# Performance work log

Hardware: AMD Instinct MI355X
Metric: run time of the kernel (lower is better)

Reference implementation:

```python
import jax, jax.numpy as jnp
import numpy as np
from jax import lax

EPS = 1e-8


def setup_inputs() -> dict:
    key = jax.random.key(0)
    ks = jax.random.split(key, 8)
    B, Cin, Cout, Wd, H, Wi, K = 16, 512, 512, 512, 64, 64, 3
    x = jax.random.normal(ks[0], (B, Cin, H, Wi), dtype=jnp.float32)
    w = jax.random.normal(ks[1], (B, Wd), dtype=jnp.float32)
    noise = jax.random.normal(ks[2], (B, 1, H, Wi), dtype=jnp.float32)
    # EqualizedLinear params (weight stored as N(0,1), runtime scale 1/sqrt(w_dim)); bias init 1.0
    w_style = jax.random.normal(ks[3], (Cin, Wd), dtype=jnp.float32)
    b_style = jnp.ones((Cin,), dtype=jnp.float32)
    # ConvModLayer equalized weight, stored N(0,1), runtime scale 1/sqrt(Cin*K*K)
    w_conv = jax.random.normal(ks[4], (Cout, Cin, K, K), dtype=jnp.float32)
    scale_noise = 0.1 * jax.random.normal(ks[5], (1,), dtype=jnp.float32)
    bias = 0.1 * jax.random.normal(ks[6], (Cout,), dtype=jnp.float32)
    return {"x": x, "w": w, "noise": noise, "w_style": w_style, "b_style": b_style,
            "w_conv": w_conv, "scale_noise": scale_noise, "bias": bias}


def reference(x, w, noise, w_style, b_style, w_conv, scale_noise, bias):
    B, Cin, H, W = x.shape
    Cout, _, K, _ = w_conv.shape
    # to_style: equalized linear, A = w @ (w_style / sqrt(w_dim)).T + b_style
    c_lin = 1.0 / jnp.sqrt(jnp.float32(w_style.shape[1]))
    A = w @ (w_style * c_lin).T + b_style  # [B, Cin]
    # modulated conv (equalized conv weight scale)
    c_conv = 1.0 / jnp.sqrt(jnp.float32(Cin * K * K))
    wts = (w_conv * c_conv)[None] * A[:, None, :, None, None]  # [B, Cout, Cin, K, K]
    demod = lax.rsqrt(jnp.sum(wts * wts, axis=(2, 3, 4), keepdims=True) + EPS)
    wts = wts * demod
    # grouped-conv batch trick: groups = B
    xg = x.reshape(1, B * Cin, H, W)
    wg = wts.reshape(B * Cout, Cin, K, K)
    out = lax.conv_general_dilated(xg, wg, (1, 1), 'SAME',
                                   feature_group_count=B,
                                   dimension_numbers=('NCHW', 'OIHW', 'NCHW'))
    out = out.reshape(B, Cout, H, W)
    out = out + scale_noise[None, :, None, None] * noise
    out = out + bias[None, :, None, None]
    return jnp.where(out >= 0, out, 0.2 * out)  # LeakyReLU(0.2)
```

## Files before the change

### kernel.cpp

```cpp
#include <hip/hip_runtime.h>
#include <stdint.h>


typedef __attribute__((ext_vector_type(8))) short s16x8;
typedef __attribute__((ext_vector_type(4))) float f32x4;

constexpr int CIN = 512, COUT = 512, WD = 512, HW = 4096;
constexpr float C_LIN  = 0.04419417382415922f;
constexpr float C_CONV = 0.014731391274719739f;
constexpr float CC2    = 1.0f / 4608.0f;

constexpr size_t WS_A = 0, WS_S = 32768, WS_DM = 1081344;
constexpr size_t WS_WP = 1310720, WS_XT = 6291456;

__device__ __forceinline__ unsigned short f2bf(float f) {
  union { float f; unsigned int u; } v; v.f = f;
  unsigned int u = v.u + 0x7FFFu + ((v.u >> 16) & 1u);
  return (unsigned short)(u >> 16);
}

__device__ __forceinline__ void gload16(const void* g, void* l) {
  __builtin_amdgcn_global_load_lds((const __attribute__((address_space(1))) void*)g,
                                   (__attribute__((address_space(3))) void*)l, 16, 0, 0);
}

__global__ void k_style(const float* __restrict__ w, const float* __restrict__ wsty,
                        const float* __restrict__ bs, float* __restrict__ A) {
  __shared__ float wl[WD];
  __shared__ float red[256];
  const int ci0 = blockIdx.x * 64, b = blockIdx.y, tid = threadIdx.x;
  for (int i = tid; i < WD; i += 256) wl[i] = w[b * WD + i];
  __syncthreads();
  const int ci_l = tid & 63, part = tid >> 6;
  const float4* row = (const float4*)(wsty + (size_t)(ci0 + ci_l) * WD + part * 128);
  float acc = 0.f;
#pragma unroll
  for (int k = 0; k < 32; ++k) {
    float4 v = row[k];
    acc += v.x * wl[part*128 + 4*k] + v.y * wl[part*128 + 4*k+1]
         + v.z * wl[part*128 + 4*k+2] + v.w * wl[part*128 + 4*k+3];
  }
  red[tid] = acc;
  __syncthreads();
  if (part == 0)
    A[b * CIN + ci0 + ci_l] =
        (red[ci_l] + red[64+ci_l] + red[128+ci_l] + red[192+ci_l]) * C_LIN + bs[ci0 + ci_l];
}

__global__ void k_s2(const float* __restrict__ w_conv, float* __restrict__ S) {
  const int co = blockIdx.x, ci = threadIdx.x;
  const float* p = w_conv + ((size_t)co * CIN + ci) * 9;
  float s = 0.f;
#pragma unroll
  for (int t = 0; t < 9; ++t) { float v = p[t]; s += v * v; }
  S[co * CIN + ci] = s;
}

__global__ void k_demod(const float* __restrict__ S, const float* __restrict__ A,
                        float* __restrict__ dm) {
  __shared__ float a2[CIN];
  __shared__ float red[256];
  const int co0 = blockIdx.x * 32, b = blockIdx.y, tid = threadIdx.x;
  for (int i = tid; i < CIN; i += 256) { float a = A[b * CIN + i]; a2[i] = a * a; }
  __syncthreads();
  const int co_l = tid & 31, part = tid >> 5;
  const float4* row = (const float4*)(S + (size_t)(co0 + co_l) * CIN + part * 64);
  float acc = 0.f;
#pragma unroll
  for (int k = 0; k < 16; ++k) {
    float4 v = row[k];
    acc += v.x * a2[part*64 + 4*k] + v.y * a2[part*64 + 4*k+1]
         + v.z * a2[part*64 + 4*k+2] + v.w * a2[part*64 + 4*k+3];
  }
  red[tid] = acc;
  __syncthreads();
  if (tid < 32) {
    float s_ = 0.f;
#pragma unroll
    for (int p = 0; p < 8; ++p) s_ += red[p * 32 + tid];
    dm[b * COUT + co0 + tid] = rsqrtf(CC2 * s_ + 1e-8f);
  }
}

__global__ void k_wpack(const float* __restrict__ wc, uint4* __restrict__ wp) {
  __shared__ float wt[64][289];
  const int ct = blockIdx.x, ch = blockIdx.y, tid = threadIdx.x;
  const int co0 = ct * 64, ci0 = ch * 32;
  for (int i = tid; i < 64 * 288; i += 256) {
    int co = i / 288, r = i - co * 288;
    wt[co][r] = wc[(size_t)(co0 + co) * 4608 + (size_t)ci0 * 9 + r];
  }
  __syncthreads();
  uint4* seg = wp + (size_t)(ct * 16 + ch) * 2304;
  for (int c = tid; c < 2304; c += 256) {
    int t = c >> 8, rem = c & 255, s = rem >> 6, co = rem & 63;
    union { unsigned short u[8]; uint4 v; } pk;
#pragma unroll
    for (int j = 0; j < 8; ++j) pk.u[j] = f2bf(wt[co][(s*8 + j) * 9 + t] * C_CONV);
    seg[c] = pk.v;
  }
}

__global__ void k_xt(const float* __restrict__ x, const float* __restrict__ A,
                     uint4* __restrict__ xt) {
  __shared__ float tile[32][132];
  __shared__ float As[32];
  const int ch = blockIdx.x, b = blockIdx.y, tid = threadIdx.x;
  const int ci0 = ch * 32;
  if (tid < 32) As[tid] = A[b * CIN + ci0 + tid];
  uint4* dst = xt + (size_t)(b * 16 + ch) * 16896;
  for (int i = tid; i < 256; i += 256) {
    int row = i >> 2, s = i & 3;
    uint4 z = {0, 0, 0, 0};
    dst[(row * 4 + s) * 66] = z;
    dst[(row * 4 + s) * 66 + 65] = z;
  }
  __syncthreads();
  for (int pt = 0; pt < 32; ++pt) {
    for (int i = tid; i < 4096; i += 256) {
      int ci = i >> 7, px = i & 127;
      tile[ci][px] = x[((size_t)(b * CIN + ci0 + ci)) * HW + pt * 128 + px] * As[ci];
    }
    __syncthreads();
    for (int c2 = tid; c2 < 512; c2 += 256) {
      int s = c2 >> 7, px = c2 & 127, rl = px >> 6, col = px & 63, row = pt * 2 + rl;
      union { unsigned short u[8]; uint4 v; } pk;
#pragma unroll
      for (int j = 0; j < 8; ++j) pk.u[j] = f2bf(tile[s*8 + j][px]);
      dst[(row * 4 + s) * 66 + 1 + col] = pk.v;
    }
    __syncthreads();
  }
}

__global__ __launch_bounds__(512, 4) void k_conv(
    const uint4* __restrict__ xt, const uint4* __restrict__ wp,
    const float* __restrict__ demod, const float* __restrict__ noise,
    const float* __restrict__ sn_, const float* __restrict__ bias,
    float* __restrict__ out) {

  __shared__ __align__(16) uint4 x_lds[2640];
  __shared__ __align__(16) uint4 w_lds[2304];
  __shared__ float dm_l[64], bi_l[64];

  const int sp = blockIdx.x, ct = blockIdx.y, b = blockIdx.z;
  const int r0 = sp * 8, co0 = ct * 64;
  const int tid = threadIdx.x, lane = tid & 63, wave = tid >> 6;
  const int l15 = lane & 15, l4 = lane >> 4;

  if (tid < 64) dm_l[tid] = demod[b * COUT + co0 + tid];
  else if (tid < 128) bi_l[tid - 64] = bias[co0 + tid - 64];
  if (sp == 0) for (int i = tid; i < 264; i += 512) x_lds[i] = (uint4){0, 0, 0, 0};
  if (sp == 7) for (int i = tid; i < 264; i += 512) x_lds[2376 + i] = (uint4){0, 0, 0, 0};

  const int lo = (r0 - 1 > 0) ? r0 - 1 : 0;
  const int hi = (r0 + 8 < 63) ? r0 + 8 : 63;
  const int cells = (hi - lo + 1) * 264;
  const int dst0 = (lo - (r0 - 1)) * 264;
  const int nI = cells >> 6, tail = cells & 63;

  f32x4 acc[4][4];
#pragma unroll
  for (int m = 0; m < 4; ++m)
#pragma unroll
    for (int f = 0; f < 4; ++f) acc[m][f] = (f32x4){0.f, 0.f, 0.f, 0.f};
  __syncthreads();

  for (int ch = 0; ch < 16; ++ch) {
    const uint4* xsrc = xt + ((size_t)(b * 16 + ch) * 64 + lo) * 264;
    const uint4* wsrc = wp + (size_t)(ct * 16 + ch) * 2304;
    for (int i = wave; i < nI; i += 8)
      gload16(xsrc + i * 64 + lane, &x_lds[dst0 + i * 64]);
    if (tid < tail) x_lds[dst0 + nI * 64 + tid] = xsrc[nI * 64 + tid];
    for (int i = wave; i < 36; i += 8)
      gload16(wsrc + i * 64 + lane, &w_lds[i * 64]);
    __syncthreads();

#pragma unroll
    for (int t = 0; t < 9; ++t) {
      const int dh = t / 3, dw = t - dh * 3;
      s16x8 afr[4], bfr[4];
#pragma unroll
      for (int m = 0; m < 4; ++m)
        afr[m] = *(const s16x8*)&w_lds[(t * 4 + l4) * 64 + m * 16 + l15];
#pragma unroll
      for (int f = 0; f < 4; ++f)
        bfr[f] = *(const s16x8*)&x_lds[((wave + dh) * 4 + l4) * 66 + f * 16 + l15 + dw];
#pragma unroll
      for (int m = 0; m < 4; ++m)
#pragma unroll
        for (int f = 0; f < 4; ++f)
          acc[m][f] = __builtin_amdgcn_mfma_f32_16x16x32_bf16(afr[m], bfr[f], acc[m][f], 0, 0, 0);
    }
    __syncthreads();
  }

  const float sn = sn_[0];
  const int row = r0 + wave;
  float nz[4];
#pragma unroll
  for (int f = 0; f < 4; ++f) nz[f] = sn * noise[b * HW + row * 64 + f * 16 + l15];
#pragma unroll
  for (int m = 0; m < 4; ++m) {
#pragma unroll
    for (int reg = 0; reg < 4; ++reg) {
      const int co_l = m * 16 + l4 * 4 + reg;
      const float d = dm_l[co_l], bv = bi_l[co_l];
      float* op = out + ((size_t)(b * COUT + co0 + co_l)) * HW + row * 64;
#pragma unroll
      for (int f = 0; f < 4; ++f) {
        float v = d * acc[m][f][reg] + nz[f] + bv;
        op[f * 16 + l15] = (v >= 0.f) ? v : 0.2f * v;
      }
    }
  }
}

extern "C" void kernel_launch(void* const* d_in, const int* in_sizes, int n_in,
                              void* d_out, int out_size, void* d_ws, size_t ws_size,
                              hipStream_t stream) {
  (void)in_sizes; (void)n_in; (void)out_size; (void)ws_size;
  const float* x           = (const float*)d_in[0];
  const float* w           = (const float*)d_in[1];
  const float* noise       = (const float*)d_in[2];
  const float* w_style     = (const float*)d_in[3];
  const float* b_style     = (const float*)d_in[4];
  const float* w_conv      = (const float*)d_in[5];
  const float* scale_noise = (const float*)d_in[6];
  const float* bias        = (const float*)d_in[7];
  float* out = (float*)d_out;

  char* ws = (char*)d_ws;
  float* A     = (float*)(ws + WS_A);
  float* S     = (float*)(ws + WS_S);
  float* demod = (float*)(ws + WS_DM);
  uint4* wpack = (uint4*)(ws + WS_WP);
  uint4* xt    = (uint4*)(ws + WS_XT);

  k_style<<<dim3(8, 16), 256, 0, stream>>>(w, w_style, b_style, A);
  k_s2<<<512, 512, 0, stream>>>(w_conv, S);
  k_demod<<<dim3(16, 16), 256, 0, stream>>>(S, A, demod);
  k_wpack<<<dim3(8, 16), 256, 0, stream>>>(w_conv, wpack);
  k_xt<<<dim3(16, 16), 256, 0, stream>>>(x, A, xt);
  k_conv<<<dim3(8, 8, 16), 512, 0, stream>>>(xt, wpack, demod, noise, scale_noise, bias, out);
}
```

Measured before the change: 499.5 us.

## Fuse weight sum-of-squares into packing, parallelize x transform, pad weight LDS rows

Merges the per-(co,ci) squared-weight sum into the weight packing kernel so w_conv is read once, removing one launch. Rewrites the x transpose/modulate kernel to use one wave per (batch, channel chunk, row) over 4096 blocks instead of 256 blocks looping over 32 tiles with LDS staging. Pads packed weight rows from 64 to 66 entries so A-fragment LDS reads in the conv use a shifted bank pattern. The padding adds a little LDS and global footprint, and the new x kernel reads x with strided per-channel loads.

```diff
diff --git a/kernel.cpp b/kernel.cpp
--- a/kernel.cpp
+++ b/kernel.cpp
@@ -9,6 +9,8 @@
 constexpr float C_LIN  = 0.04419417382415922f;
 constexpr float C_CONV = 0.014731391274719739f;
 constexpr float CC2    = 1.0f / 4608.0f;
+
+constexpr int WSEG = 2432;
 
 constexpr size_t WS_A = 0, WS_S = 32768, WS_DM = 1081344;
 constexpr size_t WS_WP = 1310720, WS_XT = 6291456;
@@ -47,13 +49,31 @@
         (red[ci_l] + red[64+ci_l] + red[128+ci_l] + red[192+ci_l]) * C_LIN + bs[ci0 + ci_l];
 }
 
-__global__ void k_s2(const float* __restrict__ w_conv, float* __restrict__ S) {
-  const int co = blockIdx.x, ci = threadIdx.x;
-  const float* p = w_conv + ((size_t)co * CIN + ci) * 9;
-  float s = 0.f;
-#pragma unroll
-  for (int t = 0; t < 9; ++t) { float v = p[t]; s += v * v; }
-  S[co * CIN + ci] = s;
+__global__ void k_sw(const float* __restrict__ wc, uint4* __restrict__ wp,
+                     float* __restrict__ S) {
+  __shared__ float wt[64][289];
+  const int ct = blockIdx.x, ch = blockIdx.y, tid = threadIdx.x;
+  const int co0 = ct * 64, ci0 = ch * 32;
+  for (int i = tid; i < 64 * 288; i += 256) {
+    int co = i / 288, r = i - co * 288;
+    wt[co][r] = wc[(size_t)(co0 + co) * 4608 + (size_t)ci0 * 9 + r];
+  }
+  __syncthreads();
+  uint4* seg = wp + (size_t)(ct * 16 + ch) * WSEG;
+  for (int c = tid; c < 2304; c += 256) {
+    int t = c >> 8, rem = c & 255, s = rem >> 6, co = rem & 63;
+    union { unsigned short u[8]; uint4 v; } pk;
+#pragma unroll
+    for (int j = 0; j < 8; ++j) pk.u[j] = f2bf(wt[co][(s*8 + j) * 9 + t] * C_CONV);
+    seg[(t * 4 + s) * 66 + co] = pk.v;
+  }
+  for (int i = tid; i < 2048; i += 256) {
+    int co = i >> 5, ci = i & 31;
+    float s_ = 0.f;
+#pragma unroll
+    for (int t = 0; t < 9; ++t) { float v = wt[co][ci * 9 + t]; s_ += v * v; }
+    S[(size_t)(co0 + co) * CIN + ci0 + ci] = s_;
+  }
 }
 
 __global__ void k_demod(const float* __restrict__ S, const float* __restrict__ A,
@@ -82,54 +102,22 @@
   }
 }
 
-__global__ void k_wpack(const float* __restrict__ wc, uint4* __restrict__ wp) {
-  __shared__ float wt[64][289];
-  const int ct = blockIdx.x, ch = blockIdx.y, tid = threadIdx.x;
-  const int co0 = ct * 64, ci0 = ch * 32;
-  for (int i = tid; i < 64 * 288; i += 256) {
-    int co = i / 288, r = i - co * 288;
-    wt[co][r] = wc[(size_t)(co0 + co) * 4608 + (size_t)ci0 * 9 + r];
-  }
-  __syncthreads();
-  uint4* seg = wp + (size_t)(ct * 16 + ch) * 2304;
-  for (int c = tid; c < 2304; c += 256) {
-    int t = c >> 8, rem = c & 255, s = rem >> 6, co = rem & 63;
-    union { unsigned short u[8]; uint4 v; } pk;
-#pragma unroll
-    for (int j = 0; j < 8; ++j) pk.u[j] = f2bf(wt[co][(s*8 + j) * 9 + t] * C_CONV);
-    seg[c] = pk.v;
-  }
-}
-
 __global__ void k_xt(const float* __restrict__ x, const float* __restrict__ A,
                      uint4* __restrict__ xt) {
-  __shared__ float tile[32][132];
-  __shared__ float As[32];
-  const int ch = blockIdx.x, b = blockIdx.y, tid = threadIdx.x;
-  const int ci0 = ch * 32;
-  if (tid < 32) As[tid] = A[b * CIN + ci0 + tid];
-  uint4* dst = xt + (size_t)(b * 16 + ch) * 16896;
-  for (int i = tid; i < 256; i += 256) {
-    int row = i >> 2, s = i & 3;
-    uint4 z = {0, 0, 0, 0};
-    dst[(row * 4 + s) * 66] = z;
-    dst[(row * 4 + s) * 66 + 65] = z;
-  }
-  __syncthreads();
-  for (int pt = 0; pt < 32; ++pt) {
-    for (int i = tid; i < 4096; i += 256) {
-      int ci = i >> 7, px = i & 127;
-      tile[ci][px] = x[((size_t)(b * CIN + ci0 + ci)) * HW + pt * 128 + px] * As[ci];
-    }
-    __syncthreads();
-    for (int c2 = tid; c2 < 512; c2 += 256) {
-      int s = c2 >> 7, px = c2 & 127, rl = px >> 6, col = px & 63, row = pt * 2 + rl;
-      union { unsigned short u[8]; uint4 v; } pk;
-#pragma unroll
-      for (int j = 0; j < 8; ++j) pk.u[j] = f2bf(tile[s*8 + j][px]);
-      dst[(row * 4 + s) * 66 + 1 + col] = pk.v;
-    }
-    __syncthreads();
+  const int wid = (blockIdx.x << 2) + (threadIdx.x >> 6);
+  const int lane = threadIdx.x & 63;
+  const int row = wid & 63, ch = (wid >> 6) & 15, b = wid >> 10;
+  const float* xb = x + ((size_t)(b * CIN + ch * 32) << 12) + (row << 6) + lane;
+  const float* Ab = A + b * CIN + ch * 32;
+  uint4* dst = xt + (size_t)((b << 4) + ch) * 16896 + (size_t)(row << 2) * 66;
+#pragma unroll
+  for (int s = 0; s < 4; ++s) {
+    union { unsigned short u[8]; uint4 v; } pk;
+#pragma unroll
+    for (int j = 0; j < 8; ++j)
+      pk.u[j] = f2bf(xb[(size_t)(s * 8 + j) << 12] * Ab[s * 8 + j]);
+    dst[s * 66 + 1 + lane] = pk.v;
+    if (lane < 2) dst[s * 66 + lane * 65] = (uint4){0, 0, 0, 0};
   }
 }
 
@@ -140,7 +128,7 @@
     float* __restrict__ out) {
 
   __shared__ __align__(16) uint4 x_lds[2640];
-  __shared__ __align__(16) uint4 w_lds[2304];
+  __shared__ __align__(16) uint4 w_lds[WSEG];
   __shared__ float dm_l[64], bi_l[64];
 
   const int sp = blockIdx.x, ct = blockIdx.y, b = blockIdx.z;
@@ -168,11 +156,11 @@
 
   for (int ch = 0; ch < 16; ++ch) {
     const uint4* xsrc = xt + ((size_t)(b * 16 + ch) * 64 + lo) * 264;
-    const uint4* wsrc = wp + (size_t)(ct * 16 + ch) * 2304;
+    const uint4* wsrc = wp + (size_t)(ct * 16 + ch) * WSEG;
     for (int i = wave; i < nI; i += 8)
       gload16(xsrc + i * 64 + lane, &x_lds[dst0 + i * 64]);
     if (tid < tail) x_lds[dst0 + nI * 64 + tid] = xsrc[nI * 64 + tid];
-    for (int i = wave; i < 36; i += 8)
+    for (int i = wave; i < 38; i += 8)
       gload16(wsrc + i * 64 + lane, &w_lds[i * 64]);
     __syncthreads();
 
@@ -182,7 +170,7 @@
       s16x8 afr[4], bfr[4];
 #pragma unroll
       for (int m = 0; m < 4; ++m)
-        afr[m] = *(const s16x8*)&w_lds[(t * 4 + l4) * 64 + m * 16 + l15];
+        afr[m] = *(const s16x8*)&w_lds[(t * 4 + l4) * 66 + m * 16 + l15];
 #pragma unroll
       for (int f = 0; f < 4; ++f)
         bfr[f] = *(const s16x8*)&x_lds[((wave + dh) * 4 + l4) * 66 + f * 16 + l15 + dw];
@@ -238,9 +226,8 @@
   uint4* xt    = (uint4*)(ws + WS_XT);
 
   k_style<<<dim3(8, 16), 256, 0, stream>>>(w, w_style, b_style, A);
-  k_s2<<<512, 512, 0, stream>>>(w_conv, S);
+  k_sw<<<dim3(8, 16), 256, 0, stream>>>(w_conv, wpack, S);
   k_demod<<<dim3(16, 16), 256, 0, stream>>>(S, A, demod);
-  k_wpack<<<dim3(8, 16), 256, 0, stream>>>(w_conv, wpack);
-  k_xt<<<dim3(16, 16), 256, 0, stream>>>(x, A, xt);
+  k_xt<<<4096, 256, 0, stream>>>(x, A, xt);
   k_conv<<<dim3(8, 8, 16), 512, 0, stream>>>(xt, wpack, demod, noise, scale_noise, bias, out);
 }
```

After: 494.5 us. About the same (-1.0%).
